# Kernel optimization log

Hardware: AMD Instinct MI355X
Metric: run time of the kernel (lower is better)

The kernel has to match this reference:

```python
import jax, jax.numpy as jnp
import numpy as np
from numpy.polynomial import Polynomial

H = 1.0    # knot spacing (init arg h)
T0 = 0.0   # left endpoint (init arg t0)
N_SAMPLES = 131072
N_KNOTS = 2048
Q = 3      # spline order -> q+1 local basis polynomials


def build_basis(h: float, q: int):
    # Faithful port of the torch module's recursive B-spline basis construction.
    o = Polynomial([0.0]); e = Polynomial([1.0]); x = Polynomial([0.0, 1.0])
    B = np.empty((q + 1, q + 1), dtype=object)
    for i in range(q + 1):
        for j in range(q + 1):
            B[i, j] = o
    B[0, 0] = e
    for p in range(1, q + 1):
        for i in range(p + 1):
            B[p, i] += B[p - 1, i] * x
            if i:
                B[p, i] += B[p - 1, i - 1](x - h) * (h * (p + 1) - x)
            B[p, i] /= h * p
    return [B[-1, i] for i in range(q + 1)]


def basis_coeff_matrix(h: float, q: int) -> np.ndarray:
    # Matches buffer_from_polynomes('B', ...): rows are polynomes[::-1],
    # coefficients in ascending power order (Polynomial.coef convention).
    polys = build_basis(h, q)
    M = np.zeros((q + 1, q + 1), dtype=np.float32)
    for j, poly in enumerate(polys[::-1]):
        c = np.asarray(poly.coef, dtype=np.float64)
        M[j, :len(c)] = c.astype(np.float32)
    return M


def setup_inputs() -> dict:
    key = jax.random.key(0)
    # samples inside the spline support so most knot indices are in-range
    xs = jax.random.uniform(key, (N_SAMPLES,), dtype=jnp.float32,
                            minval=0.0, maxval=(N_KNOTS - Q) * H)
    B = jnp.asarray(basis_coeff_matrix(H, Q))  # [q+1, q+1]
    return {"xs": xs, "B": B, "n": N_KNOTS, "q": Q}


def reference(xs, B, n, q):
    # xs: [N] float32, B: [q+1, q+1] ascending-power coeffs, n/q: python ints
    x = xs - T0
    first_i = jnp.floor(x / H).astype(jnp.int32)          # [N] knot bin index
    offs = jnp.arange(q + 1)
    cols = first_i[:, None] + offs[None, :]               # [N, q+1]
    # local coordinate for each of the q+1 overlapping basis polynomials
    x_loc = (x - first_i.astype(xs.dtype) * H)[:, None] + H * (q - offs)[None, :].astype(xs.dtype)
    # power series 0..q, then dot with coefficient rows: values[n,k] = sum_p x_loc^p * B[k,p]
    powers = x_loc[:, :, None] ** jnp.arange(q + 1)       # [N, q+1, q+1]
    values = jnp.einsum('nkp,kp->nk', powers, B)          # [N, q+1]
    valid = (cols >= 0) & (cols < n)
    cols_c = jnp.clip(cols, 0, n - 1)
    rows = jnp.arange(xs.shape[0])[:, None]
    out = jnp.zeros((xs.shape[0], n), dtype=xs.dtype)
    out = out.at[rows, cols_c].add(jnp.where(valid, values, jnp.zeros_like(values)))
    return out
```

## Files before the change

### kernel.cpp

```cpp
#include <hip/hip_runtime.h>


constexpr int BLOCK = 256;
constexpr int ROWS_PER_BLOCK = 32;

typedef float floatx4 __attribute__((ext_vector_type(4)));

__global__ __launch_bounds__(BLOCK) void bspline_fill_kernel(
    const float* __restrict__ xs,
    const float* __restrict__ B,
    float* __restrict__ out,
    int n_samples,
    int n_knots) {
    const int tid = threadIdx.x;
    const int base_row = blockIdx.x * ROWS_PER_BLOCK;
    const int rows = min(ROWS_PER_BLOCK, n_samples - base_row);

    float x = 0.0f;
    if (tid < rows) x = xs[base_row + tid];

    float* chunk = out + (size_t)base_row * (size_t)n_knots;
    const size_t nfloats = (size_t)rows * (size_t)n_knots;

    const size_t nvec = nfloats & ~(size_t)3;
    const floatx4 z = {0.0f, 0.0f, 0.0f, 0.0f};
    for (size_t f = (size_t)tid * 4; f < nvec; f += (size_t)BLOCK * 4) {
        __builtin_nontemporal_store(z, (floatx4*)(chunk + f));
    }
    for (size_t f = nvec + (size_t)tid; f < nfloats; f += (size_t)BLOCK) {
        chunk[f] = 0.0f;
    }

    __syncthreads();

    if (tid < rows) {
        const float fif = floorf(x);
        const int fi = (int)fif;
        const float frac = x - fif;
        float t, v0, v1, v2, v3;
        t = frac + 3.0f; v0 = ((B[ 3]*t + B[ 2])*t + B[ 1])*t + B[ 0];
        t = frac + 2.0f; v1 = ((B[ 7]*t + B[ 6])*t + B[ 5])*t + B[ 4];
        t = frac + 1.0f; v2 = ((B[11]*t + B[10])*t + B[ 9])*t + B[ 8];
        t = frac;        v3 = ((B[15]*t + B[14])*t + B[13])*t + B[12];
        const float vals[4] = {v0, v1, v2, v3};
        float* rowp = chunk + (size_t)tid * (size_t)n_knots;
        #pragma unroll
        for (int k = 0; k < 4; ++k) {
            const int c = fi + k;
            if (c >= 0 && c < n_knots) rowp[c] = vals[k];
        }
    }
}

extern "C" void kernel_launch(void* const* d_in, const int* in_sizes, int n_in,
                              void* d_out, int out_size, void* d_ws, size_t ws_size,
                              hipStream_t stream) {
    const float* xs = (const float*)d_in[0];
    const float* B  = (const float*)d_in[1];
    float* out = (float*)d_out;

    const int n_samples = in_sizes[0];
    const int n_knots   = out_size / n_samples;

    const int grid = (n_samples + ROWS_PER_BLOCK - 1) / ROWS_PER_BLOCK;
    bspline_fill_kernel<<<grid, BLOCK, 0, stream>>>(xs, B, out, n_samples, n_knots);
}
```

Before: 1.068 ms.

## Split zero-fill and scatter into separate kernels with grid-stride fill

Replaces the per-block fused zero-fill plus barrier plus scatter with two kernels: a grid-stride vectorised zero fill over the whole output and a one-thread-per-row scatter of the four basis values. This removes the intra-block barrier and the nontemporal stores, and lets the fill run as a pure streaming write. It adds a second launch and drops the scalar tail handling for sizes not divisible by four.

```diff
diff --git a/kernel.cpp b/kernel.cpp
--- a/kernel.cpp
+++ b/kernel.cpp
@@ -2,53 +2,44 @@
 
 
 constexpr int BLOCK = 256;
-constexpr int ROWS_PER_BLOCK = 32;
 
 typedef float floatx4 __attribute__((ext_vector_type(4)));
 
-__global__ __launch_bounds__(BLOCK) void bspline_fill_kernel(
+__global__ __launch_bounds__(BLOCK) void zero_fill_kernel(
+    float* __restrict__ out, size_t nvec4) {
+    const floatx4 z = {0.0f, 0.0f, 0.0f, 0.0f};
+    const size_t stride = (size_t)gridDim.x * BLOCK;
+    floatx4* p = (floatx4*)out;
+    for (size_t i = (size_t)blockIdx.x * BLOCK + threadIdx.x; i < nvec4; i += stride) {
+        p[i] = z;
+    }
+}
+
+__global__ __launch_bounds__(BLOCK) void scatter_kernel(
     const float* __restrict__ xs,
     const float* __restrict__ B,
     float* __restrict__ out,
     int n_samples,
     int n_knots) {
-    const int tid = threadIdx.x;
-    const int base_row = blockIdx.x * ROWS_PER_BLOCK;
-    const int rows = min(ROWS_PER_BLOCK, n_samples - base_row);
+    const int row = blockIdx.x * BLOCK + threadIdx.x;
+    if (row >= n_samples) return;
+    const float x = xs[row];
+    const float fif = floorf(x);
+    const int fi = (int)fif;
+    const float frac = x - fif;
 
-    float x = 0.0f;
-    if (tid < rows) x = xs[base_row + tid];
+    float t, v0, v1, v2, v3;
+    t = frac + 3.0f; v0 = ((B[ 3]*t + B[ 2])*t + B[ 1])*t + B[ 0];
+    t = frac + 2.0f; v1 = ((B[ 7]*t + B[ 6])*t + B[ 5])*t + B[ 4];
+    t = frac + 1.0f; v2 = ((B[11]*t + B[10])*t + B[ 9])*t + B[ 8];
+    t = frac;        v3 = ((B[15]*t + B[14])*t + B[13])*t + B[12];
 
-    float* chunk = out + (size_t)base_row * (size_t)n_knots;
-    const size_t nfloats = (size_t)rows * (size_t)n_knots;
-
-    const size_t nvec = nfloats & ~(size_t)3;
-    const floatx4 z = {0.0f, 0.0f, 0.0f, 0.0f};
-    for (size_t f = (size_t)tid * 4; f < nvec; f += (size_t)BLOCK * 4) {
-        __builtin_nontemporal_store(z, (floatx4*)(chunk + f));
-    }
-    for (size_t f = nvec + (size_t)tid; f < nfloats; f += (size_t)BLOCK) {
-        chunk[f] = 0.0f;
-    }
-
-    __syncthreads();
-
-    if (tid < rows) {
-        const float fif = floorf(x);
-        const int fi = (int)fif;
-        const float frac = x - fif;
-        float t, v0, v1, v2, v3;
-        t = frac + 3.0f; v0 = ((B[ 3]*t + B[ 2])*t + B[ 1])*t + B[ 0];
-        t = frac + 2.0f; v1 = ((B[ 7]*t + B[ 6])*t + B[ 5])*t + B[ 4];
-        t = frac + 1.0f; v2 = ((B[11]*t + B[10])*t + B[ 9])*t + B[ 8];
-        t = frac;        v3 = ((B[15]*t + B[14])*t + B[13])*t + B[12];
-        const float vals[4] = {v0, v1, v2, v3};
-        float* rowp = chunk + (size_t)tid * (size_t)n_knots;
-        #pragma unroll
-        for (int k = 0; k < 4; ++k) {
-            const int c = fi + k;
-            if (c >= 0 && c < n_knots) rowp[c] = vals[k];
-        }
+    float* rowp = out + (size_t)row * (size_t)n_knots;
+    const float vals[4] = {v0, v1, v2, v3};
+    #pragma unroll
+    for (int k = 0; k < 4; ++k) {
+        const int c = fi + k;
+        if (c >= 0 && c < n_knots) rowp[c] = vals[k];
     }
 }
 
@@ -62,6 +53,11 @@
     const int n_samples = in_sizes[0];
     const int n_knots   = out_size / n_samples;
 
-    const int grid = (n_samples + ROWS_PER_BLOCK - 1) / ROWS_PER_BLOCK;
-    bspline_fill_kernel<<<grid, BLOCK, 0, stream>>>(xs, B, out, n_samples, n_knots);
+    const size_t nfloats = (size_t)n_samples * (size_t)n_knots;
+    const size_t nvec4 = nfloats / 4;
+
+    zero_fill_kernel<<<2048, BLOCK, 0, stream>>>(out, nvec4);
+
+    const int grid_b = (n_samples + BLOCK - 1) / BLOCK;
+    scatter_kernel<<<grid_b, BLOCK, 0, stream>>>(xs, B, out, n_samples, n_knots);
 }
```

New measurement: 1.120 ms. +4.9%, slower.
